# Performance work log

Measured on AMD Instinct MI355X. Metric: run time of the kernel, lower is better.

The kernel has to match this reference:

```python
import jax, jax.numpy as jnp
import numpy as np

D_MODEL = 1024
NUM_HEADS = 16
HEAD_DIM = D_MODEL // NUM_HEADS


def setup_inputs() -> dict:
    key = jax.random.key(0)
    ks = jax.random.split(key, 9)
    s = 1.0 / np.sqrt(D_MODEL)  # torch Linear default init range scale
    def lin(k):
        kw, kb = jax.random.split(k)
        W = jax.random.uniform(kw, (D_MODEL, D_MODEL), jnp.float32, -s, s)
        b = jax.random.uniform(kb, (D_MODEL,), jnp.float32, -s, s)
        return W, b
    Wq, bq = lin(ks[0])
    Wk, bk = lin(ks[1])
    Wv, bv = lin(ks[2])
    Wo, bo = lin(ks[3])
    x = jax.random.normal(ks[4], (4, 2048, D_MODEL), jnp.float32)
    return {"x": x, "Wq": Wq, "bq": bq, "Wk": Wk, "bk": bk,
            "Wv": Wv, "bv": bv, "Wo": Wo, "bo": bo}


def reference(x, Wq, bq, Wk, bk, Wv, bv, Wo, bo):
    B, S, _ = x.shape
    H, Dh = NUM_HEADS, HEAD_DIM
    scale = Dh ** -0.5
    # projections; W stored as [in, out] so y = x @ W + b
    q = (x @ Wq + bq).reshape(B, S, H, Dh).transpose(0, 2, 1, 3)  # [B,H,S,Dh]
    k = (x @ Wk + bk).reshape(B, S, H, Dh).transpose(0, 2, 1, 3)
    v = (x @ Wv + bv).reshape(B, S, H, Dh).transpose(0, 2, 1, 3)
    scores = jnp.einsum('bhqd,bhkd->bhqk', q, k) * scale  # [B,H,S,S]
    causal = jnp.tril(jnp.ones((S, S), dtype=bool))
    scores = jnp.where(causal[None, None], scores, jnp.finfo(scores.dtype).min)
    attn = jax.nn.softmax(scores, axis=-1)
    out = jnp.einsum('bhqk,bhkd->bhqd', attn, v)  # [B,H,S,Dh]
    out = out.transpose(0, 2, 1, 3).reshape(B, S, H * Dh)
    return out @ Wo + bo
```

## Files before the change

kernel.cpp:

```cpp
#include <hip/hip_runtime.h>
#include <math.h>

#define DM 1024
#define NH 16
#define DH 64
#define BB 4
#define SS 2048
#define MROWS (BB*SS)

typedef __bf16 bf16;
typedef __bf16 bf16x2 __attribute__((ext_vector_type(2)));
typedef __bf16 bf16x8 __attribute__((ext_vector_type(8)));
typedef float floatx4 __attribute__((ext_vector_type(4)));
typedef unsigned int uintx4 __attribute__((ext_vector_type(4)));
typedef unsigned int uintx2 __attribute__((ext_vector_type(2)));

#if __has_builtin(__builtin_amdgcn_exp2f)
#define EXP2F __builtin_amdgcn_exp2f
#else
#define EXP2F exp2f
#endif

#define QSCALE (0.125f * 1.44269504088896f)

__device__ __forceinline__ void cp16(void* lds, const void* g) {
  __builtin_amdgcn_global_load_lds(
      (__attribute__((address_space(1))) void*)(void*)g,
      (__attribute__((address_space(3))) void*)lds,
      16, 0, 0);
}

__device__ __forceinline__ unsigned pk2(float a, float b) {
  bf16x2 t;
  t[0] = (bf16)a;
  t[1] = (bf16)b;
  return __builtin_bit_cast(unsigned, t);
}

#if __has_builtin(__builtin_amdgcn_permlane32_swap) && \
    __has_builtin(__builtin_amdgcn_permlane16_swap)
__device__ __forceinline__ void pl32(unsigned& a, unsigned& b) {
  uintx2 r = __builtin_amdgcn_permlane32_swap(a, b, false, false);
  a = r[0]; b = r[1];
}
__device__ __forceinline__ void pl16(unsigned& a, unsigned& b) {
  uintx2 r = __builtin_amdgcn_permlane16_swap(a, b, false, false);
  a = r[0]; b = r[1];
}
#else
__device__ __forceinline__ void pl32(unsigned& a, unsigned& b) {
  asm volatile("v_permlane32_swap_b32 %0, %1" : "+v"(a), "+v"(b));
}
__device__ __forceinline__ void pl16(unsigned& a, unsigned& b) {
  asm volatile("v_permlane16_swap_b32 %0, %1" : "+v"(a), "+v"(b));
}
#endif

__global__ __launch_bounds__(256) void cvt_x(
    const float* __restrict__ X, bf16* __restrict__ Y) {
  int i = (blockIdx.x * 256 + threadIdx.x) * 8;
  float4 a = *(const float4*)&X[i];
  float4 b = *(const float4*)&X[i + 4];
  bf16x8 o;
  o[0] = (bf16)a.x; o[1] = (bf16)a.y; o[2] = (bf16)a.z; o[3] = (bf16)a.w;
  o[4] = (bf16)b.x; o[5] = (bf16)b.y; o[6] = (bf16)b.z; o[7] = (bf16)b.w;
  *(bf16x8*)&Y[i] = o;
}

__global__ __launch_bounds__(1024) void wtransc(
    const float* __restrict__ W0, const float* __restrict__ W1,
    const float* __restrict__ W2, const float* __restrict__ W3,
    bf16* __restrict__ T0, bf16* __restrict__ T1,
    bf16* __restrict__ T2, bf16* __restrict__ T3) {
  __shared__ float tile[32][33];
  const float* W; bf16* T;
  int z = blockIdx.z;
  if (z == 0)      { W = W0; T = T0; }
  else if (z == 1) { W = W1; T = T1; }
  else if (z == 2) { W = W2; T = T2; }
  else             { W = W3; T = T3; }
  int tx = threadIdx.x, ty = threadIdx.y;
  tile[ty][tx] = W[(blockIdx.y * 32 + ty) * DM + blockIdx.x * 32 + tx];
  __syncthreads();
  T[(blockIdx.x * 32 + ty) * DM + blockIdx.y * 32 + tx] = (bf16)tile[tx][ty];
}

#define BK 32

__global__ __launch_bounds__(512, 1) void gemm_qkv(
    const bf16* __restrict__ A, const bf16* __restrict__ WT,
    const float* __restrict__ bq, const float* __restrict__ bk,
    const float* __restrict__ bv,
    bf16* __restrict__ qb, bf16* __restrict__ kb, bf16* __restrict__ vt) {
  __shared__ __align__(16) char smem[(2 * 256 * 64 + 2 * 128 * 64) * 2];
  bf16* Ab = (bf16*)smem;
  bf16* Bb = (bf16*)(smem + 2 * 256 * 64 * 2);
  bf16* Ts = (bf16*)smem;

  int tid = threadIdx.x;
  int lane = tid & 63, w = tid >> 6;
  int wr = w >> 1, wc = w & 1;
  int qd = lane >> 4, l15 = lane & 15;

  int bid = blockIdx.x;
  int wg = (bid & 7) * 96 + (bid >> 3);
  int mb = wg / 24, nb = wg % 24;
  int m0 = mb * 256;
  int n0 = nb * 128;
  int which = n0 >> 10;

  floatx4 acc[4][4] = {};

  auto stageA = [&](int pb, int t, int hf) {
    for (int i = 0; i < 2; ++i) {
      int L = i * 512 + tid;
      int row = L >> 3, ch = L & 7;
      int sch = ch ^ (row & 7);
      cp16(&Ab[pb * 256 * 64 + (hf * 128 + row) * 64 + ch * 8],
           &A[(size_t)(m0 + hf * 128 + row) * DM + t * 64 + sch * 8]);
    }
  };
  auto stageB = [&](int pb, int t) {
    for (int i = 0; i < 2; ++i) {
      int L = i * 512 + tid;
      int row = L >> 3, ch = L & 7;
      int sch = ch ^ (row & 7);
      cp16(&Bb[pb * 128 * 64 + row * 64 + ch * 8],
           &WT[(size_t)(n0 + row) * DM + t * 64 + sch * 8]);
    }
  };
  auto ldA = [&](int pb, int mt, int ks) -> bf16x8 {
    int row = wr * 64 + mt * 16 + l15;
    int c = ((ks << 2) + qd) ^ (row & 7);
    return *(const bf16x8*)&Ab[pb * 256 * 64 + row * 64 + c * 8];
  };
  auto ldB = [&](int pb, int nt, int ks) -> bf16x8 {
    int row = wc * 64 + nt * 16 + l15;
    int c = ((ks << 2) + qd) ^ (row & 7);
    return *(const bf16x8*)&Bb[pb * 128 * 64 + row * 64 + c * 8];
  };

  stageA(0, 0, 0);
  stageA(0, 0, 1);
  stageB(0, 0);
  stageB(1, 1);
  asm volatile("s_waitcnt vmcnt(2)" ::: "memory");
  __builtin_amdgcn_s_barrier();

  for (int g = 0; g < 16; ++g) {
    int pb = g & 1;
    bf16x8 af0[2][2], bfr[4][2];
    for (int mt = 0; mt < 2; ++mt)
      for (int ks = 0; ks < 2; ++ks) af0[mt][ks] = ldA(pb, mt, ks);
    for (int nt = 0; nt < 4; ++nt)
      for (int ks = 0; ks < 2; ++ks) bfr[nt][ks] = ldB(pb, nt, ks);
    if (g + 1 < 16) { stageA(pb ^ 1, g + 1, 0); stageA(pb ^ 1, g + 1, 1); }
    __builtin_amdgcn_s_barrier();
    asm volatile("s_waitcnt lgkmcnt(0)" ::: "memory");
    __builtin_amdgcn_sched_barrier(0);
    __builtin_amdgcn_s_setprio(1);
    for (int mt = 0; mt < 2; ++mt)
      for (int nt = 0; nt < 4; ++nt)
        for (int ks = 0; ks < 2; ++ks)
          acc[mt][nt] = __builtin_amdgcn_mfma_f32_16x16x32_bf16(
              af0[mt][ks], bfr[nt][ks], acc[mt][nt], 0, 0, 0);
    __builtin_amdgcn_s_setprio(0);
    __builtin_amdgcn_s_barrier();
    bf16x8 af1[2][2];
    for (int mt = 0; mt < 2; ++mt)
      for (int ks = 0; ks < 2; ++ks) af1[mt][ks] = ldA(pb, 2 + mt, ks);
    if (g + 2 < 16) stageB(pb, g + 2);
    __builtin_amdgcn_s_barrier();
    asm volatile("s_waitcnt lgkmcnt(0)" ::: "memory");
    __builtin_amdgcn_sched_barrier(0);
    __builtin_amdgcn_s_setprio(1);
    for (int mt = 0; mt < 2; ++mt)
      for (int nt = 0; nt < 4; ++nt)
        for (int ks = 0; ks < 2; ++ks)
          acc[2 + mt][nt] = __builtin_amdgcn_mfma_f32_16x16x32_bf16(
              af1[mt][ks], bfr[nt][ks], acc[2 + mt][nt], 0, 0, 0);
    __builtin_amdgcn_s_setprio(0);
    if (g < 14)
      asm volatile("s_waitcnt vmcnt(2)" ::: "memory");
    else if (g == 14)
      asm volatile("s_waitcnt vmcnt(0)" ::: "memory");
    __builtin_amdgcn_s_barrier();
  }

  __syncthreads();

  const float* bias = (which == 0) ? bq : (which == 1) ? bk : bv;

  if (which == 2) {
    for (int nt = 0; nt < 4; ++nt) {
      int dl = wc * 64 + nt * 16 + l15;
      float bv_ = bias[(n0 & 1023) + dl];
      for (int mt = 0; mt < 4; ++mt)
        for (int r = 0; r < 4; ++r)
          Ts[dl * 264 + wr * 64 + mt * 16 + qd * 4 + r] =
              (bf16)(acc[mt][nt][r] + bv_);
    }
    __syncthreads();
    int dl = tid >> 2, s0 = (tid & 3) * 64;
    size_t vrow = (size_t)((n0 & 1023) + dl) * MROWS + m0 + s0;
    for (int j = 0; j < 8; ++j)
      *(bf16x8*)&vt[vrow + j * 8] = *(const bf16x8*)&Ts[dl * 264 + s0 + j * 8];
  } else {
    bf16* out = (which == 0) ? qb : kb;
    float sc = (which == 0) ? QSCALE : 1.0f;
    for (int nt = 0; nt < 4; ++nt) {
      int col = (n0 & 1023) + wc * 64 + nt * 16 + l15;
      float bv_ = bias[col];
      for (int mt = 0; mt < 4; ++mt)
        for (int r = 0; r < 4; ++r) {
          int row = m0 + wr * 64 + mt * 16 + qd * 4 + r;
          out[(size_t)row * DM + col] = (bf16)((acc[mt][nt][r] + bv_) * sc);
        }
    }
  }
}

__global__ __launch_bounds__(256, 4) void gemm_out(
    const bf16* __restrict__ A, const bf16* __restrict__ WT,
    const float* __restrict__ bias, float* __restrict__ C) {
  __shared__ __align__(16) bf16 As[2][64 * BK];
  __shared__ __align__(16) bf16 Bs[2][128 * BK];
  int tid = threadIdx.x;
  int lane = tid & 63, w = tid >> 6;
  int wm = (w >> 1) * 32;
  int wn = (w & 1) * 64;
  int m0 = blockIdx.x * 64;
  int n0 = blockIdx.y * 128;
  int qd = lane >> 4;
  int l15 = lane & 15;

  floatx4 acc[2][4] = {};

  auto stage = [&](int pb, int k0) {
    {
      int ci = w * 64;
      int c = ci + lane;
      int r = c >> 2, cc = (c & 3) * 8;
      cp16(&As[pb][ci * 8], &A[(size_t)(m0 + r) * DM + k0 + cc]);
    }
    for (int i = 0; i < 2; ++i) {
      int ci = (w * 2 + i) * 64;
      int c = ci + lane;
      int r = c >> 2, cc = (c & 3) * 8;
      cp16(&Bs[pb][ci * 8], &WT[(size_t)(n0 + r) * DM + k0 + cc]);
    }
  };

  stage(0, 0);
  __syncthreads();

  for (int t = 0; t < DM / BK; ++t) {
    int pb = t & 1;
    if (t + 1 < DM / BK) stage(pb ^ 1, (t + 1) * BK);
    bf16x8 af[2], bfr[4];
    for (int mt = 0; mt < 2; ++mt)
      af[mt] = *(const bf16x8*)&As[pb][(wm + mt * 16 + l15) * BK + qd * 8];
    for (int nt = 0; nt < 4; ++nt)
      bfr[nt] = *(const bf16x8*)&Bs[pb][(wn + nt * 16 + l15) * BK + qd * 8];
    for (int mt = 0; mt < 2; ++mt)
      for (int nt = 0; nt < 4; ++nt)
        acc[mt][nt] = __builtin_amdgcn_mfma_f32_16x16x32_bf16(
            af[mt], bfr[nt], acc[mt][nt], 0, 0, 0);
    __syncthreads();
  }

  for (int nt = 0; nt < 4; ++nt) {
    int col = n0 + wn + nt * 16 + l15;
    float bv = bias[col];
    for (int mt = 0; mt < 2; ++mt)
      for (int r = 0; r < 4; ++r) {
        int row = m0 + wm + mt * 16 + qd * 4 + r;
        C[(size_t)row * DM + col] = acc[mt][nt][r] + bv;
      }
  }
}

__global__ __launch_bounds__(512, 4) void attn_fwd(
    const bf16* __restrict__ Qg, const bf16* __restrict__ Kg,
    const bf16* __restrict__ Vt, bf16* __restrict__ O) {
  __shared__ __align__(16) bf16 Kbuf[3][64 * 64];
  __shared__ __align__(16) bf16 Vbuf[3][64 * 64];

  int tid = threadIdx.x;
  int lane = tid & 63, w = tid >> 6;
  int qd = lane >> 4, l15 = lane & 15;
  int sw = l15 & 7;
  int pair = blockIdx.x, h = blockIdx.y, b = blockIdx.z;
  int base = b * SS;
  int hoff = h * DH;

  int gch = ((lane & 7) ^ (lane >> 3)) * 8;
  auto stage = [&](int bi, int kt) {
    int kbase = base + kt * 64;
    int ci = w * 64;
    int row = (ci + lane) >> 3;
    cp16(&Kbuf[bi][ci * 8], &Kg[(size_t)(kbase + row) * DM + hoff + gch]);
    cp16(&Vbuf[bi][ci * 8],
         &Vt[(size_t)(hoff + row) * MROWS + base + kt * 64 + gch]);
  };

  for (int ph = 0; ph < 2; ++ph) {
    int qt = ph ? (15 - pair) : pair;
    int q0 = qt * 128;
    int nkt = 2 * qt + 2;

    stage(0, 0);
    stage(1, 1);

    bf16x8 qf[2];
    {
      int qrow = base + q0 + w * 16 + l15;
      for (int ks = 0; ks < 2; ++ks)
        qf[ks] = *(const bf16x8*)&Qg[(size_t)qrow * DM + hoff + ks * 32 + qd * 8];
    }

    float m_r = -3e38f;
    float lacc = 0.0f;
    floatx4 oacc[4] = {};

    asm volatile("s_waitcnt vmcnt(4)" ::: "memory");
    __builtin_amdgcn_s_barrier();

    int bi = 0;
    for (int kt = 0; kt < nkt; ++kt) {
      if (kt + 2 < nkt) stage((bi + 2) % 3, kt + 2);

      floatx4 s[4] = {};
      for (int ks = 0; ks < 2; ++ks)
        for (int nt = 0; nt < 4; ++nt) {
          bf16x8 kf = *(const bf16x8*)
              &Kbuf[bi][(nt * 16 + l15) * 64 + (((ks << 2) + qd) ^ sw) * 8];
          s[nt] = __builtin_amdgcn_mfma_f32_16x16x32_bf16(
              kf, qf[ks], s[nt], 0, 0, 0);
        }

      int rowq = q0 + w * 16 + l15;
      if (kt >= 2 * qt) {
        for (int nt = 0; nt < 4; ++nt)
          for (int r = 0; r < 4; ++r) {
            int col = kt * 64 + nt * 16 + qd * 4 + r;
            if (col > rowq) s[nt][r] = -3e38f;
          }
      }

      floatx4 m4 = s[0];
      for (int nt = 1; nt < 4; ++nt)
        for (int r = 0; r < 4; ++r) m4[r] = fmaxf(m4[r], s[nt][r]);
      float t = fmaxf(fmaxf(m4[0], m4[1]), fmaxf(m4[2], m4[3]));
      t = fmaxf(t, __shfl_xor(t, 16, 64));
      t = fmaxf(t, __shfl_xor(t, 32, 64));

      if (!__all(t <= m_r + 11.0f)) {
        float mn = fmaxf(m_r, t);
        float al = EXP2F(m_r - mn);
        m_r = mn;
        for (int dt = 0; dt < 4; ++dt)
          for (int r = 0; r < 4; ++r) oacc[dt][r] *= al;
        lacc *= al;
      }

      bf16x8 pf[2];
      for (int ks = 0; ks < 2; ++ks) {
        float pu[4], pv[4];
        for (int r = 0; r < 4; ++r) {
          pu[r] = EXP2F(s[2 * ks][r] - m_r);
          pv[r] = EXP2F(s[2 * ks + 1][r] - m_r);
        }
        lacc += ((pu[0] + pu[1]) + (pu[2] + pu[3])) +
                ((pv[0] + pv[1]) + (pv[2] + pv[3]));
        unsigned u0 = pk2(pu[0], pu[1]), u1 = pk2(pu[2], pu[3]);
        unsigned v0 = pk2(pv[0], pv[1]), v1 = pk2(pv[2], pv[3]);
        pl32(u0, v0); pl16(u0, v0);
        pl32(u1, v1); pl16(u1, v1);
        uintx4 ww;
        ww[0] = u0; ww[1] = u1; ww[2] = v0; ww[3] = v1;
        pf[ks] = __builtin_bit_cast(bf16x8, ww);
      }

      for (int ks = 0; ks < 2; ++ks)
        for (int dt = 0; dt < 4; ++dt) {
          bf16x8 vf = *(const bf16x8*)
              &Vbuf[bi][(dt * 16 + l15) * 64 + (((ks << 2) + qd) ^ sw) * 8];
          oacc[dt] = __builtin_amdgcn_mfma_f32_16x16x32_bf16(
              pf[ks], vf, oacc[dt], 0, 0, 0);
        }

      int rem = nkt - 1 - kt;
      if (rem >= 2) {
        asm volatile("s_waitcnt vmcnt(2)" ::: "memory");
        __builtin_amdgcn_s_barrier();
      } else if (rem == 1) {
        asm volatile("s_waitcnt vmcnt(0)" ::: "memory");
        __builtin_amdgcn_s_barrier();
      }
      bi = (bi == 2) ? 0 : bi + 1;
    }

    __syncthreads();

    lacc += __shfl_xor(lacc, 16, 64);
    lacc += __shfl_xor(lacc, 32, 64);
    for (int r = 0; r < 4; ++r) {
      float inv = 1.0f / __shfl(lacc, qd * 4 + r, 64);
      int row = base + q0 + w * 16 + qd * 4 + r;
      for (int dt = 0; dt < 4; ++dt)
        O[(size_t)row * DM + hoff + dt * 16 + l15] = (bf16)(oacc[dt][r] * inv);
    }
  }
}

extern "C" void kernel_launch(void* const* d_in, const int* in_sizes, int n_in,
                              void* d_out, int out_size, void* d_ws, size_t ws_size,
                              hipStream_t stream) {
  const float* x  = (const float*)d_in[0];
  const float* Wq = (const float*)d_in[1];
  const float* bq = (const float*)d_in[2];
  const float* Wk = (const float*)d_in[3];
  const float* bk = (const float*)d_in[4];
  const float* Wv = (const float*)d_in[5];
  const float* bv = (const float*)d_in[6];
  const float* Wo = (const float*)d_in[7];
  const float* bo = (const float*)d_in[8];
  float* out = (float*)d_out;

  char* ws = (char*)d_ws;
  const size_t act = (size_t)MROWS * DM * sizeof(bf16);
  bf16* xb    = (bf16*)(ws);
  bf16* qb    = (bf16*)(ws + act);
  bf16* kb    = (bf16*)(ws + 2 * act);
  bf16* vt    = (bf16*)(ws + 3 * act);
  bf16* ab    = (bf16*)(ws + 4 * act);
  bf16* WqkvT = (bf16*)(ws + 5 * act);
  bf16* WoT   = WqkvT + 3 * (size_t)DM * DM;

  cvt_x<<<MROWS * DM / (256 * 8), 256, 0, stream>>>(x, xb);
  wtransc<<<dim3(32, 32, 4), dim3(32, 32), 0, stream>>>(
      Wq, Wk, Wv, Wo,
      WqkvT, WqkvT + (size_t)DM * DM, WqkvT + 2 * (size_t)DM * DM, WoT);

  gemm_qkv<<<768, 512, 0, stream>>>(
      xb, WqkvT, bq, bk, bv, qb, kb, vt);

  attn_fwd<<<dim3(8, NH, BB), 512, 0, stream>>>(qb, kb, vt, ab);

  gemm_out<<<dim3(128, 8), 256, 0, stream>>>(ab, WoT, bo, out);
}
```

Baseline: 270.9 us.

## Switch attention to 32x32x16 MFMA with 256-row query tiles per block

```diff
diff --git a/kernel.cpp b/kernel.cpp
--- a/kernel.cpp
+++ b/kernel.cpp
@@ -12,6 +12,7 @@
 typedef __bf16 bf16x2 __attribute__((ext_vector_type(2)));
 typedef __bf16 bf16x8 __attribute__((ext_vector_type(8)));
 typedef float floatx4 __attribute__((ext_vector_type(4)));
+typedef float floatx16 __attribute__((ext_vector_type(16)));
 typedef unsigned int uintx4 __attribute__((ext_vector_type(4)));
 typedef unsigned int uintx2 __attribute__((ext_vector_type(2)));
 
@@ -37,22 +38,14 @@
   return __builtin_bit_cast(unsigned, t);
 }
 
-#if __has_builtin(__builtin_amdgcn_permlane32_swap) && \
-    __has_builtin(__builtin_amdgcn_permlane16_swap)
+#if __has_builtin(__builtin_amdgcn_permlane32_swap)
 __device__ __forceinline__ void pl32(unsigned& a, unsigned& b) {
   uintx2 r = __builtin_amdgcn_permlane32_swap(a, b, false, false);
   a = r[0]; b = r[1];
 }
-__device__ __forceinline__ void pl16(unsigned& a, unsigned& b) {
-  uintx2 r = __builtin_amdgcn_permlane16_swap(a, b, false, false);
-  a = r[0]; b = r[1];
-}
 #else
 __device__ __forceinline__ void pl32(unsigned& a, unsigned& b) {
   asm volatile("v_permlane32_swap_b32 %0, %1" : "+v"(a), "+v"(b));
-}
-__device__ __forceinline__ void pl16(unsigned& a, unsigned& b) {
-  asm volatile("v_permlane16_swap_b32 %0, %1" : "+v"(a), "+v"(b));
 }
 #endif
 
@@ -280,7 +273,7 @@
   }
 }
 
-__global__ __launch_bounds__(512, 4) void attn_fwd(
+__global__ __launch_bounds__(512, 2) void attn_fwd(
     const bf16* __restrict__ Qg, const bf16* __restrict__ Kg,
     const bf16* __restrict__ Vt, bf16* __restrict__ O) {
   __shared__ __align__(16) bf16 Kbuf[3][64 * 64];
@@ -288,13 +281,12 @@
 
   int tid = threadIdx.x;
   int lane = tid & 63, w = tid >> 6;
-  int qd = lane >> 4, l15 = lane & 15;
-  int sw = l15 & 7;
+  int q31 = lane & 31, hi = lane >> 5;
   int pair = blockIdx.x, h = blockIdx.y, b = blockIdx.z;
   int base = b * SS;
   int hoff = h * DH;
 
-  int gch = ((lane & 7) ^ (lane >> 3)) * 8;
+  int gch = ((lane & 7) ^ ((lane >> 3) & 7)) * 8;
   auto stage = [&](int bi, int kt) {
     int kbase = base + kt * 64;
     int ci = w * 64;
@@ -304,24 +296,25 @@
          &Vt[(size_t)(hoff + row) * MROWS + base + kt * 64 + gch]);
   };
 
+  int swz = q31 & 7;
+
   for (int ph = 0; ph < 2; ++ph) {
-    int qt = ph ? (15 - pair) : pair;
-    int q0 = qt * 128;
-    int nkt = 2 * qt + 2;
+    int jt = ph ? (7 - pair) : pair;
+    int q0 = jt * 256;
+    int nkt = 4 * (jt + 1);
 
     stage(0, 0);
     stage(1, 1);
 
-    bf16x8 qf[2];
-    {
-      int qrow = base + q0 + w * 16 + l15;
-      for (int ks = 0; ks < 2; ++ks)
-        qf[ks] = *(const bf16x8*)&Qg[(size_t)qrow * DM + hoff + ks * 32 + qd * 8];
-    }
+    int rowq = q0 + w * 32 + q31;
+    bf16x8 qf[4];
+    for (int ds = 0; ds < 4; ++ds)
+      qf[ds] = *(const bf16x8*)
+          &Qg[(size_t)(base + rowq) * DM + hoff + ds * 16 + hi * 8];
 
     float m_r = -3e38f;
     float lacc = 0.0f;
-    floatx4 oacc[4] = {};
+    floatx16 oacc0 = {}, oacc1 = {};
 
     asm volatile("s_waitcnt vmcnt(4)" ::: "memory");
     __builtin_amdgcn_s_barrier();
@@ -330,65 +323,90 @@
     for (int kt = 0; kt < nkt; ++kt) {
       if (kt + 2 < nkt) stage((bi + 2) % 3, kt + 2);
 
-      floatx4 s[4] = {};
-      for (int ks = 0; ks < 2; ++ks)
-        for (int nt = 0; nt < 4; ++nt) {
-          bf16x8 kf = *(const bf16x8*)
-              &Kbuf[bi][(nt * 16 + l15) * 64 + (((ks << 2) + qd) ^ sw) * 8];
-          s[nt] = __builtin_amdgcn_mfma_f32_16x16x32_bf16(
-              kf, qf[ks], s[nt], 0, 0, 0);
+      floatx16 sA = {}, sB = {};
+      for (int ds = 0; ds < 4; ++ds) {
+        bf16x8 kfA = *(const bf16x8*)
+            &Kbuf[bi][(q31)*64 + (((ds << 1) + hi) ^ swz) * 8];
+        bf16x8 kfB = *(const bf16x8*)
+            &Kbuf[bi][(32 + q31) * 64 + (((ds << 1) + hi) ^ swz) * 8];
+        sA = __builtin_amdgcn_mfma_f32_32x32x16_bf16(kfA, qf[ds], sA, 0, 0, 0);
+        sB = __builtin_amdgcn_mfma_f32_32x32x16_bf16(kfB, qf[ds], sB, 0, 0, 0);
+      }
+
+      if (kt >= 4 * jt) {
+#pragma unroll
+        for (int r = 0; r < 16; ++r) {
+          int key = kt * 64 + (r & 3) + 8 * (r >> 2) + 4 * hi;
+          if (key > rowq) sA[r] = -3e38f;
+          if (key + 32 > rowq) sB[r] = -3e38f;
         }
-
-      int rowq = q0 + w * 16 + l15;
-      if (kt >= 2 * qt) {
-        for (int nt = 0; nt < 4; ++nt)
-          for (int r = 0; r < 4; ++r) {
-            int col = kt * 64 + nt * 16 + qd * 4 + r;
-            if (col > rowq) s[nt][r] = -3e38f;
-          }
-      }
-
-      floatx4 m4 = s[0];
-      for (int nt = 1; nt < 4; ++nt)
-        for (int r = 0; r < 4; ++r) m4[r] = fmaxf(m4[r], s[nt][r]);
-      float t = fmaxf(fmaxf(m4[0], m4[1]), fmaxf(m4[2], m4[3]));
-      t = fmaxf(t, __shfl_xor(t, 16, 64));
+      }
+
+      float t0 = sA[0], t1 = sA[1], t2 = sB[0], t3 = sB[1];
+#pragma unroll
+      for (int r = 2; r < 16; r += 2) {
+        t0 = fmaxf(t0, sA[r]); t1 = fmaxf(t1, sA[r + 1]);
+        t2 = fmaxf(t2, sB[r]); t3 = fmaxf(t3, sB[r + 1]);
+      }
+      float t = fmaxf(fmaxf(t0, t1), fmaxf(t2, t3));
       t = fmaxf(t, __shfl_xor(t, 32, 64));
 
       if (!__all(t <= m_r + 11.0f)) {
         float mn = fmaxf(m_r, t);
         float al = EXP2F(m_r - mn);
         m_r = mn;
-        for (int dt = 0; dt < 4; ++dt)
-          for (int r = 0; r < 4; ++r) oacc[dt][r] *= al;
+#pragma unroll
+        for (int r = 0; r < 16; ++r) { oacc0[r] *= al; oacc1[r] *= al; }
         lacc *= al;
       }
 
-      bf16x8 pf[2];
-      for (int ks = 0; ks < 2; ++ks) {
-        float pu[4], pv[4];
-        for (int r = 0; r < 4; ++r) {
-          pu[r] = EXP2F(s[2 * ks][r] - m_r);
-          pv[r] = EXP2F(s[2 * ks + 1][r] - m_r);
-        }
-        lacc += ((pu[0] + pu[1]) + (pu[2] + pu[3])) +
-                ((pv[0] + pv[1]) + (pv[2] + pv[3]));
-        unsigned u0 = pk2(pu[0], pu[1]), u1 = pk2(pu[2], pu[3]);
-        unsigned v0 = pk2(pv[0], pv[1]), v1 = pk2(pv[2], pv[3]);
-        pl32(u0, v0); pl16(u0, v0);
-        pl32(u1, v1); pl16(u1, v1);
-        uintx4 ww;
-        ww[0] = u0; ww[1] = u1; ww[2] = v0; ww[3] = v1;
-        pf[ks] = __builtin_bit_cast(bf16x8, ww);
-      }
-
-      for (int ks = 0; ks < 2; ++ks)
-        for (int dt = 0; dt < 4; ++dt) {
-          bf16x8 vf = *(const bf16x8*)
-              &Vbuf[bi][(dt * 16 + l15) * 64 + (((ks << 2) + qd) ^ sw) * 8];
-          oacc[dt] = __builtin_amdgcn_mfma_f32_16x16x32_bf16(
-              pf[ks], vf, oacc[dt], 0, 0, 0);
-        }
+      float pA[16], pB[16];
+#pragma unroll
+      for (int r = 0; r < 16; ++r) {
+        pA[r] = EXP2F(sA[r] - m_r);
+        pB[r] = EXP2F(sB[r] - m_r);
+      }
+      float s0 = 0.f, s1 = 0.f, s2 = 0.f, s3 = 0.f;
+#pragma unroll
+      for (int r = 0; r < 16; r += 2) {
+        s0 += pA[r]; s1 += pA[r + 1];
+        s2 += pB[r]; s3 += pB[r + 1];
+      }
+      lacc += (s0 + s1) + (s2 + s3);
+
+      bf16x8 pf[4];
+      {
+        unsigned w0 = pk2(pA[0], pA[1]), w2 = pk2(pA[4], pA[5]);
+        unsigned w1 = pk2(pA[2], pA[3]), w3 = pk2(pA[6], pA[7]);
+        pl32(w0, w2); pl32(w1, w3);
+        uintx4 ww; ww[0] = w0; ww[1] = w1; ww[2] = w2; ww[3] = w3;
+        pf[0] = __builtin_bit_cast(bf16x8, ww);
+        w0 = pk2(pA[8], pA[9]);  w2 = pk2(pA[12], pA[13]);
+        w1 = pk2(pA[10], pA[11]); w3 = pk2(pA[14], pA[15]);
+        pl32(w0, w2); pl32(w1, w3);
+        ww[0] = w0; ww[1] = w1; ww[2] = w2; ww[3] = w3;
+        pf[1] = __builtin_bit_cast(bf16x8, ww);
+        w0 = pk2(pB[0], pB[1]);  w2 = pk2(pB[4], pB[5]);
+        w1 = pk2(pB[2], pB[3]);  w3 = pk2(pB[6], pB[7]);
+        pl32(w0, w2); pl32(w1, w3);
+        ww[0] = w0; ww[1] = w1; ww[2] = w2; ww[3] = w3;
+        pf[2] = __builtin_bit_cast(bf16x8, ww);
+        w0 = pk2(pB[8], pB[9]);  w2 = pk2(pB[12], pB[13]);
+        w1 = pk2(pB[10], pB[11]); w3 = pk2(pB[14], pB[15]);
+        pl32(w0, w2); pl32(w1, w3);
+        ww[0] = w0; ww[1] = w1; ww[2] = w2; ww[3] = w3;
+        pf[3] = __builtin_bit_cast(bf16x8, ww);
+      }
+
+#pragma unroll
+      for (int s4 = 0; s4 < 4; ++s4) {
+        bf16x8 vf0 = *(const bf16x8*)
+            &Vbuf[bi][(q31)*64 + (((s4 << 1) + hi) ^ swz) * 8];
+        bf16x8 vf1 = *(const bf16x8*)
+            &Vbuf[bi][(32 + q31) * 64 + (((s4 << 1) + hi) ^ swz) * 8];
+        oacc0 = __builtin_amdgcn_mfma_f32_32x32x16_bf16(pf[s4], vf0, oacc0, 0, 0, 0);
+        oacc1 = __builtin_amdgcn_mfma_f32_32x32x16_bf16(pf[s4], vf1, oacc1, 0, 0, 0);
+      }
 
       int rem = nkt - 1 - kt;
       if (rem >= 2) {
@@ -403,13 +421,14 @@
 
     __syncthreads();
 
-    lacc += __shfl_xor(lacc, 16, 64);
     lacc += __shfl_xor(lacc, 32, 64);
-    for (int r = 0; r < 4; ++r) {
-      float inv = 1.0f / __shfl(lacc, qd * 4 + r, 64);
-      int row = base + q0 + w * 16 + qd * 4 + r;
-      for (int dt = 0; dt < 4; ++dt)
-        O[(size_t)row * DM + hoff + dt * 16 + l15] = (bf16)(oacc[dt][r] * inv);
+#pragma unroll
+    for (int r = 0; r < 16; ++r) {
+      int rr = (r & 3) + 8 * (r >> 2) + 4 * hi;
+      float inv = 1.0f / __shfl(lacc, rr, 64);
+      size_t row = (size_t)(base + q0 + w * 32 + rr) * DM + hoff;
+      O[row + q31] = (bf16)(oacc0[r] * inv);
+      O[row + 32 + q31] = (bf16)(oacc1[r] * inv);
     }
   }
 }
@@ -446,7 +465,7 @@
   gemm_qkv<<<768, 512, 0, stream>>>(
       xb, WqkvT, bq, bk, bv, qb, kb, vt);
 
-  attn_fwd<<<dim3(8, NH, BB), 512, 0, stream>>>(qb, kb, vt, ab);
+  attn_fwd<<<dim3(4, NH, BB), 512, 0, stream>>>(qb, kb, vt, ab);
 
   gemm_out<<<dim3(128, 8), 256, 0, stream>>>(ab, WoT, bo, out);
 }
```

After: 265.6 us. No clear change (-1.9%).
